# Kernel optimization log

Hardware: AMD Instinct MI355X
Metric: run time of the kernel (lower is better)

## Reference

```python
import jax, jax.numpy as jnp
import numpy as np

E = 1024

def setup_inputs() -> dict:
    key = jax.random.key(0)
    ks = jax.random.split(key, 9)
    s = 1.0 / np.sqrt(E)
    return {
        "x": jax.random.normal(ks[0], (4, 2048, E), dtype=jnp.float32),
        "Wq": jax.random.uniform(ks[1], (E, E), jnp.float32, -s, s),
        "bq": jax.random.uniform(ks[2], (E,), jnp.float32, -s, s),
        "Wk": jax.random.uniform(ks[3], (E, E), jnp.float32, -s, s),
        "bk": jax.random.uniform(ks[4], (E,), jnp.float32, -s, s),
        "Wv": jax.random.uniform(ks[5], (E, E), jnp.float32, -s, s),
        "bv": jax.random.uniform(ks[6], (E,), jnp.float32, -s, s),
        "Wo": jax.random.uniform(ks[7], (E, E), jnp.float32, -s, s),
        "bo": jax.random.uniform(ks[8], (E,), jnp.float32, -s, s),
    }

def reference(x, Wq, bq, Wk, bk, Wv, bv, Wo, bo):
    # Note: the torch module never splits heads; attention is over full embed_dim.
    # nn.Linear: y = x @ W.T + b
    Q = jnp.einsum('bse,fe->bsf', x, Wq) + bq
    K = jnp.einsum('bse,fe->bsf', x, Wk) + bk
    V = jnp.einsum('bse,fe->bsf', x, Wv) + bv
    scale = 1.0 / jnp.sqrt(jnp.asarray(x.shape[-1], x.dtype))
    scores = jnp.einsum('bqe,bke->bqk', Q, K) * scale  # [B, S, S]
    weights = jax.nn.softmax(scores, axis=-1)
    out = jnp.einsum('bqk,bke->bqe', weights, V)
    # dropout is identity in eval mode
    return jnp.einsum('bse,fe->bsf', out, Wo) + bo
```

## Files before the change

### kernel.cpp

```cpp
#include <hip/hip_runtime.h>
#include <hip/hip_bf16.h>
#include <stdint.h>

typedef short bf16x8 __attribute__((ext_vector_type(8)));
typedef float f32x4 __attribute__((ext_vector_type(4)));
typedef __attribute__((address_space(3))) void lds_void_t;
typedef __attribute__((address_space(1))) void g_void_t;

static __device__ __forceinline__ unsigned short f2b(float f) {
    __hip_bfloat16 b = __float2bfloat16(f);
    return __builtin_bit_cast(unsigned short, b);
}
static __device__ __forceinline__ float b2f(unsigned int u) {
    return __builtin_bit_cast(float, u << 16);
}

__global__ __launch_bounds__(256) void cast_f32_bf16(
    const float* __restrict__ in, ushort* __restrict__ out, int n4)
{
    int i = blockIdx.x * blockDim.x + threadIdx.x;
    const int stride = gridDim.x * blockDim.x;
    for (; i < n4; i += stride) {
        float4 v = reinterpret_cast<const float4*>(in)[i];
        ushort4 o;
        o.x = f2b(v.x); o.y = f2b(v.y); o.z = f2b(v.z); o.w = f2b(v.w);
        reinterpret_cast<ushort4*>(out)[i] = o;
    }
}

template<typename CT, bool HAS_BIAS>
__global__ __launch_bounds__(256, 2)
void gemm_bt(const ushort* __restrict__ A, const ushort* __restrict__ B,
             const float* __restrict__ bias, CT* __restrict__ C,
             int lda, int ldb, int ldc, int K,
             long strideA, long strideB, long strideC, float alpha)
{
    __shared__ __align__(16) ushort sA[128 * 64];
    __shared__ __align__(16) ushort sB[128 * 64];

    const int bz = blockIdx.z;
    A += (size_t)bz * strideA;
    B += (size_t)bz * strideB;
    C += (size_t)bz * strideC;

    const int tid = threadIdx.x;
    const int w   = tid >> 6;
    const int l   = tid & 63;
    const int wr  = w >> 1;
    const int wc  = w & 1;

    const int bRow = blockIdx.y * 128;
    const int bCol = blockIdx.x * 128;

    const int lr   = l >> 3;
    const int scol = (((l & 7) ^ lr) << 3);

    f32x4 acc[4][4];
#pragma unroll
    for (int m = 0; m < 4; ++m)
#pragma unroll
        for (int n = 0; n < 4; ++n)
            acc[m][n] = f32x4{0.f, 0.f, 0.f, 0.f};

    for (int k0 = 0; k0 < K; k0 += 64) {
#pragma unroll
        for (int p = 0; p < 4; ++p) {
            const int c   = p * 4 + w;
            const int row = c * 8 + lr;
            const ushort* gA = A + (size_t)(bRow + row) * lda + (k0 + scol);
            const ushort* gB = B + (size_t)(bCol + row) * ldb + (k0 + scol);
            __builtin_amdgcn_global_load_lds((const g_void_t*)gA,
                (lds_void_t*)((char*)sA + c * 1024), 16, 0, 0);
            __builtin_amdgcn_global_load_lds((const g_void_t*)gB,
                (lds_void_t*)((char*)sB + c * 1024), 16, 0, 0);
        }
        __syncthreads();

        bf16x8 af[4][2], bfv[4][2];
#pragma unroll
        for (int m = 0; m < 4; ++m) {
            const int ar = wr * 64 + m * 16 + (l & 15);
#pragma unroll
            for (int ks = 0; ks < 2; ++ks) {
                const int slot = (ks * 4 + (l >> 4)) ^ (ar & 7);
                af[m][ks] = *reinterpret_cast<const bf16x8*>(
                    (const char*)sA + ar * 128 + slot * 16);
            }
        }
#pragma unroll
        for (int n = 0; n < 4; ++n) {
            const int br = wc * 64 + n * 16 + (l & 15);
#pragma unroll
            for (int ks = 0; ks < 2; ++ks) {
                const int slot = (ks * 4 + (l >> 4)) ^ (br & 7);
                bfv[n][ks] = *reinterpret_cast<const bf16x8*>(
                    (const char*)sB + br * 128 + slot * 16);
            }
        }
#pragma unroll
        for (int ks = 0; ks < 2; ++ks)
#pragma unroll
            for (int m = 0; m < 4; ++m)
#pragma unroll
                for (int n = 0; n < 4; ++n)
                    acc[m][n] = __builtin_amdgcn_mfma_f32_16x16x32_bf16(
                        af[m][ks], bfv[n][ks], acc[m][n], 0, 0, 0);
        __syncthreads();
    }

    const int cl = l & 15;
#pragma unroll
    for (int n = 0; n < 4; ++n) {
        const int col = bCol + wc * 64 + n * 16 + cl;
        const float bv = HAS_BIAS ? bias[col] : 0.f;
#pragma unroll
        for (int m = 0; m < 4; ++m) {
#pragma unroll
            for (int r = 0; r < 4; ++r) {
                const int row = bRow + wr * 64 + m * 16 + (l >> 4) * 4 + r;
                const float v = (acc[m][n][r] + bv) * alpha;
                if constexpr (sizeof(CT) == 2)
                    ((ushort*)C)[(size_t)row * ldc + col] = f2b(v);
                else
                    ((float*)C)[(size_t)row * ldc + col] = v;
            }
        }
    }
}

__global__ __launch_bounds__(256) void softmax_rows(ushort* __restrict__ S)
{
    __shared__ float red[8];
    const size_t row = blockIdx.x;
    ushort* p = S + row * 2048;
    const int tid = threadIdx.x;

    uint4 v = reinterpret_cast<uint4*>(p)[tid];
    float f[8];
    const unsigned int* wv = reinterpret_cast<const unsigned int*>(&v);
#pragma unroll
    for (int j = 0; j < 4; ++j) {
        f[2 * j]     = b2f(wv[j] & 0xFFFFu);
        f[2 * j + 1] = b2f(wv[j] >> 16);
    }
    float mx = f[0];
#pragma unroll
    for (int j = 1; j < 8; ++j) mx = fmaxf(mx, f[j]);
#pragma unroll
    for (int s = 1; s < 64; s <<= 1) mx = fmaxf(mx, __shfl_xor(mx, s));
    if ((tid & 63) == 0) red[tid >> 6] = mx;
    __syncthreads();
    mx = fmaxf(fmaxf(red[0], red[1]), fmaxf(red[2], red[3]));

    float sum = 0.f;
#pragma unroll
    for (int j = 0; j < 8; ++j) { f[j] = __expf(f[j] - mx); sum += f[j]; }
#pragma unroll
    for (int s = 1; s < 64; s <<= 1) sum += __shfl_xor(sum, s);
    if ((tid & 63) == 0) red[4 + (tid >> 6)] = sum;
    __syncthreads();
    sum = (red[4] + red[5]) + (red[6] + red[7]);
    const float inv = 1.0f / sum;

    uint4 o;
    unsigned int* wo = reinterpret_cast<unsigned int*>(&o);
#pragma unroll
    for (int j = 0; j < 4; ++j) {
        const unsigned int lo = f2b(f[2 * j] * inv);
        const unsigned int hi = f2b(f[2 * j + 1] * inv);
        wo[j] = lo | (hi << 16);
    }
    reinterpret_cast<uint4*>(p)[tid] = o;
}

__global__ __launch_bounds__(256) void transpose_v(
    const ushort* __restrict__ V, ushort* __restrict__ Vt)
{
    __shared__ ushort t[64][65];
    const int b  = blockIdx.z;
    const int e0 = blockIdx.x * 64;
    const int s0 = blockIdx.y * 64;
    const int tid = threadIdx.x;
    const int cg = (tid & 15) * 4;
    const int r0 = tid >> 4;

    const ushort* Vb = V + (size_t)b * 2048 * 1024;
#pragma unroll
    for (int p = 0; p < 4; ++p) {
        const int r = r0 + p * 16;
        ushort4 x = *reinterpret_cast<const ushort4*>(
            Vb + (size_t)(s0 + r) * 1024 + e0 + cg);
        t[r][cg + 0] = x.x; t[r][cg + 1] = x.y;
        t[r][cg + 2] = x.z; t[r][cg + 3] = x.w;
    }
    __syncthreads();
    ushort* Vtb = Vt + (size_t)b * 1024 * 2048;
#pragma unroll
    for (int p = 0; p < 4; ++p) {
        const int e = r0 + p * 16;
        ushort4 o;
        o.x = t[cg + 0][e]; o.y = t[cg + 1][e];
        o.z = t[cg + 2][e]; o.w = t[cg + 3][e];
        *reinterpret_cast<ushort4*>(Vtb + (size_t)(e0 + e) * 2048 + s0 + cg) = o;
    }
}

extern "C" void kernel_launch(void* const* d_in, const int* in_sizes, int n_in,
                              void* d_out, int out_size, void* d_ws, size_t ws_size,
                              hipStream_t stream)
{
    const float* x  = (const float*)d_in[0];
    const float* Wq = (const float*)d_in[1];
    const float* bq = (const float*)d_in[2];
    const float* Wk = (const float*)d_in[3];
    const float* bk = (const float*)d_in[4];
    const float* Wv = (const float*)d_in[5];
    const float* bv = (const float*)d_in[6];
    const float* Wo = (const float*)d_in[7];
    const float* bo = (const float*)d_in[8];

    char* ws = (char*)d_ws;
    ushort* xb  = (ushort*)(ws);
    ushort* Wqb = (ushort*)(ws + 16777216);
    ushort* Wkb = (ushort*)(ws + 18874368);
    ushort* Wvb = (ushort*)(ws + 20971520);
    ushort* Wob = (ushort*)(ws + 23068672);
    ushort* Qb  = (ushort*)(ws + 25165824);
    ushort* Kb  = (ushort*)(ws + 41943040);
    ushort* Vb  = (ushort*)(ws + 58720256);
    ushort* Vtb = (ushort*)(ws + 75497472);
    ushort* Sb  = (ushort*)(ws + 92274688);
    ushort* Ob  = (ushort*)(ws + 125829120);

    cast_f32_bf16<<<2048, 256, 0, stream>>>(x,  xb,  2097152);
    cast_f32_bf16<<<1024, 256, 0, stream>>>(Wq, Wqb, 262144);
    cast_f32_bf16<<<1024, 256, 0, stream>>>(Wk, Wkb, 262144);
    cast_f32_bf16<<<1024, 256, 0, stream>>>(Wv, Wvb, 262144);
    cast_f32_bf16<<<1024, 256, 0, stream>>>(Wo, Wob, 262144);

    gemm_bt<ushort, true><<<dim3(8, 64, 1), 256, 0, stream>>>(
        xb, Wqb, bq, Qb, 1024, 1024, 1024, 1024, 0, 0, 0, 0.03125f);
    gemm_bt<ushort, true><<<dim3(8, 64, 1), 256, 0, stream>>>(
        xb, Wkb, bk, Kb, 1024, 1024, 1024, 1024, 0, 0, 0, 1.0f);
    gemm_bt<ushort, true><<<dim3(8, 64, 1), 256, 0, stream>>>(
        xb, Wvb, bv, Vb, 1024, 1024, 1024, 1024, 0, 0, 0, 1.0f);

    transpose_v<<<dim3(16, 32, 4), 256, 0, stream>>>(Vb, Vtb);

    gemm_bt<ushort, false><<<dim3(16, 16, 4), 256, 0, stream>>>(
        Qb, Kb, nullptr, Sb, 1024, 1024, 2048, 1024,
        2048L * 1024, 2048L * 1024, 2048L * 2048, 1.0f);

    softmax_rows<<<8192, 256, 0, stream>>>(Sb);

    gemm_bt<ushort, false><<<dim3(8, 16, 4), 256, 0, stream>>>(
        Sb, Vtb, nullptr, Ob, 2048, 2048, 1024, 2048,
        2048L * 2048, 1024L * 2048, 2048L * 1024, 1.0f);

    gemm_bt<float, true><<<dim3(8, 64, 1), 256, 0, stream>>>(
        Ob, Wob, bo, (float*)d_out, 1024, 1024, 1024, 1024, 0, 0, 0, 1.0f);
}
```

Measured before the change: 315.2 us.

## Fuse QKV projections into one GEMM, add tile swizzle, raise occupancy hint

Concatenates the Wq/Wk/Wv weights and biases so the three projection GEMMs become a single wider GEMM writing an interleaved QKV buffer, and the downstream kernels read Q, K and V through strided views. The 1/sqrt(E) scale moves from the Q projection to the QK^T GEMM's alpha. The GEMM also gets an XCD-aware block remap that places consecutive tiles on the same chiplet for L2 reuse, and its launch-bounds min-blocks rises from 2 to 4. The higher occupancy hint may force register spills, and the scale now applies to the scores after they are accumulated rather than to Q before the bf16 rounding.

After: 303.5 us. 3.7% less time.

```diff
diff --git a/kernel.cpp b/kernel.cpp
--- a/kernel.cpp
+++ b/kernel.cpp
@@ -28,8 +28,17 @@
     }
 }
 
+__global__ __launch_bounds__(256) void concat_bias(
+    const float* __restrict__ b0, const float* __restrict__ b1,
+    const float* __restrict__ b2, float* __restrict__ out)
+{
+    const int i = blockIdx.x * blockDim.x + threadIdx.x;
+    const int sec = i >> 10, off = i & 1023;
+    out[i] = sec == 0 ? b0[off] : (sec == 1 ? b1[off] : b2[off]);
+}
+
 template<typename CT, bool HAS_BIAS>
-__global__ __launch_bounds__(256, 2)
+__global__ __launch_bounds__(256, 4)
 void gemm_bt(const ushort* __restrict__ A, const ushort* __restrict__ B,
              const float* __restrict__ bias, CT* __restrict__ C,
              int lda, int ldb, int ldc, int K,
@@ -42,6 +51,17 @@
     A += (size_t)bz * strideA;
     B += (size_t)bz * strideB;
     C += (size_t)bz * strideC;
+
+    const int gx = gridDim.x, gy = gridDim.y;
+    const int nwg = gx * gy;
+    int bx = blockIdx.x, by = blockIdx.y;
+    if ((nwg & 7) == 0) {
+        const int flat = blockIdx.x + gx * blockIdx.y;
+        const int cpx = nwg >> 3;
+        const int u = (flat & 7) * cpx + (flat >> 3);
+        bx = u % gx;
+        by = u / gx;
+    }
 
     const int tid = threadIdx.x;
     const int w   = tid >> 6;
@@ -49,8 +69,8 @@
     const int wr  = w >> 1;
     const int wc  = w & 1;
 
-    const int bRow = blockIdx.y * 128;
-    const int bCol = blockIdx.x * 128;
+    const int bRow = by * 128;
+    const int bCol = bx * 128;
 
     const int lr   = l >> 3;
     const int scol = (((l & 7) ^ lr) << 3);
@@ -174,7 +194,7 @@
 }
 
 __global__ __launch_bounds__(256) void transpose_v(
-    const ushort* __restrict__ V, ushort* __restrict__ Vt)
+    const ushort* __restrict__ V, ushort* __restrict__ Vt, int ldv, long strideV)
 {
     __shared__ ushort t[64][65];
     const int b  = blockIdx.z;
@@ -184,12 +204,12 @@
     const int cg = (tid & 15) * 4;
     const int r0 = tid >> 4;
 
-    const ushort* Vb = V + (size_t)b * 2048 * 1024;
+    const ushort* Vb = V + (size_t)b * strideV;
 #pragma unroll
     for (int p = 0; p < 4; ++p) {
         const int r = r0 + p * 16;
         ushort4 x = *reinterpret_cast<const ushort4*>(
-            Vb + (size_t)(s0 + r) * 1024 + e0 + cg);
+            Vb + (size_t)(s0 + r) * ldv + e0 + cg);
         t[r][cg + 0] = x.x; t[r][cg + 1] = x.y;
         t[r][cg + 2] = x.z; t[r][cg + 3] = x.w;
     }
@@ -220,36 +240,31 @@
     const float* bo = (const float*)d_in[8];
 
     char* ws = (char*)d_ws;
-    ushort* xb  = (ushort*)(ws);
-    ushort* Wqb = (ushort*)(ws + 16777216);
-    ushort* Wkb = (ushort*)(ws + 18874368);
-    ushort* Wvb = (ushort*)(ws + 20971520);
-    ushort* Wob = (ushort*)(ws + 23068672);
-    ushort* Qb  = (ushort*)(ws + 25165824);
-    ushort* Kb  = (ushort*)(ws + 41943040);
-    ushort* Vb  = (ushort*)(ws + 58720256);
-    ushort* Vtb = (ushort*)(ws + 75497472);
-    ushort* Sb  = (ushort*)(ws + 92274688);
-    ushort* Ob  = (ushort*)(ws + 125829120);
-
-    cast_f32_bf16<<<2048, 256, 0, stream>>>(x,  xb,  2097152);
-    cast_f32_bf16<<<1024, 256, 0, stream>>>(Wq, Wqb, 262144);
-    cast_f32_bf16<<<1024, 256, 0, stream>>>(Wk, Wkb, 262144);
-    cast_f32_bf16<<<1024, 256, 0, stream>>>(Wv, Wvb, 262144);
+    ushort* xb    = (ushort*)(ws);
+    ushort* Wqkvb = (ushort*)(ws + 16777216);
+    ushort* Wob   = (ushort*)(ws + 23068672);
+    float*  bqkv  = (float*) (ws + 25165824);
+    ushort* QKVb  = (ushort*)(ws + 26214400);
+    ushort* Vtb   = (ushort*)(ws + 76546048);
+    ushort* Sb    = (ushort*)(ws + 93323264);
+    ushort* Ob    = (ushort*)(ws + 126877696);
+
+    cast_f32_bf16<<<2048, 256, 0, stream>>>(x,  xb, 2097152);
+    cast_f32_bf16<<<1024, 256, 0, stream>>>(Wq, Wqkvb,           262144);
+    cast_f32_bf16<<<1024, 256, 0, stream>>>(Wk, Wqkvb + 1048576, 262144);
+    cast_f32_bf16<<<1024, 256, 0, stream>>>(Wv, Wqkvb + 2097152, 262144);
     cast_f32_bf16<<<1024, 256, 0, stream>>>(Wo, Wob, 262144);
-
-    gemm_bt<ushort, true><<<dim3(8, 64, 1), 256, 0, stream>>>(
-        xb, Wqb, bq, Qb, 1024, 1024, 1024, 1024, 0, 0, 0, 0.03125f);
-    gemm_bt<ushort, true><<<dim3(8, 64, 1), 256, 0, stream>>>(
-        xb, Wkb, bk, Kb, 1024, 1024, 1024, 1024, 0, 0, 0, 1.0f);
-    gemm_bt<ushort, true><<<dim3(8, 64, 1), 256, 0, stream>>>(
-        xb, Wvb, bv, Vb, 1024, 1024, 1024, 1024, 0, 0, 0, 1.0f);
-
-    transpose_v<<<dim3(16, 32, 4), 256, 0, stream>>>(Vb, Vtb);
+    concat_bias<<<12, 256, 0, stream>>>(bq, bk, bv, bqkv);
+
+    gemm_bt<ushort, true><<<dim3(24, 64, 1), 256, 0, stream>>>(
+        xb, Wqkvb, bqkv, QKVb, 1024, 1024, 3072, 1024, 0, 0, 0, 1.0f);
+
+    transpose_v<<<dim3(16, 32, 4), 256, 0, stream>>>(
+        QKVb + 2048, Vtb, 3072, 2048L * 3072);
 
     gemm_bt<ushort, false><<<dim3(16, 16, 4), 256, 0, stream>>>(
-        Qb, Kb, nullptr, Sb, 1024, 1024, 2048, 1024,
-        2048L * 1024, 2048L * 1024, 2048L * 2048, 1.0f);
+        QKVb, QKVb + 1024, nullptr, Sb, 3072, 3072, 2048, 1024,
+        2048L * 3072, 2048L * 3072, 2048L * 2048, 0.03125f);
 
     softmax_rows<<<8192, 256, 0, stream>>>(Sb);
 
```
